# Performance work log

Measured on AMD Instinct MI355X. Metric: run time of the kernel, lower is better.

Reference implementation:

```python
import jax, jax.numpy as jnp
import numpy as np

B, C, T, F = 64, 128, 2048, 5
ALPHA, BETA = 0.5, 0.5
N = C * F  # 640 nodes


def _spatial_adjacency():
    # |i-j| <= 3 neighbors within each frequency band block (block diagonal)
    idx = np.arange(C)
    d = np.abs(idx[:, None] - idx[None, :])
    blk = ((d <= 3) & (d > 0)).astype(np.float32)
    return jnp.asarray(np.kron(np.eye(F, dtype=np.float32), blk))


A_SPATIAL = _spatial_adjacency()  # (N, N)


def setup_inputs() -> dict:
    key = jax.random.key(0)
    ks = jax.random.split(key, 5)
    names = ['delta', 'theta', 'alpha', 'beta', 'gamma']
    return {n: jax.random.normal(k, (B, C, T), dtype=jnp.float32) for n, k in zip(names, ks)}


def _strg(delta, theta, alpha, beta, gamma):
    bands = jnp.stack([delta, theta, alpha, beta, gamma], axis=1)  # (B, F, C, T)
    Bn, Fn, Cn, Tn = bands.shape

    # bandpower = unbiased variance over time (torch.var default ddof=1)
    bp = jnp.var(bands, axis=3, ddof=1)  # (B, F, C)
    bandpowers = jnp.transpose(bp, (0, 2, 1))  # (B, C, F)
    # node ordering: node f*C + ch -> bandpowers[b, ch, f] == bp[b, f, ch]
    node_features = bp.reshape(Bn, Fn * Cn, 1)

    # Pearson-style functional connectivity per batch & band (vectorized)
    mean = jnp.mean(bands, axis=3, keepdims=True)
    std = jnp.std(bands, axis=3, ddof=1, keepdims=True)  # torch.std unbiased
    xn = (bands - mean) / (std + 1e-8)
    corr = jnp.einsum('bfct,bfdt->bfcd', xn, xn) / (Tn - 1)  # (B, F, C, C)
    corr = jnp.abs(corr)
    eye = jnp.eye(Cn, dtype=corr.dtype)
    corr = corr * (1.0 - eye) + eye  # zero diag, then set diag = 1
    corr = 0.5 * (corr + jnp.swapaxes(corr, 2, 3))

    # block-diagonal assembly into full functional adjacency
    A_func = jnp.zeros((Bn, N, N), dtype=corr.dtype)
    for f in range(Fn):
        s = f * Cn
        A_func = A_func.at[:, s:s + Cn, s:s + Cn].set(corr[:, f])

    A = ALPHA * A_SPATIAL[None] + BETA * A_func  # (B, N, N)

    # symmetric degree normalization D^-1/2 A D^-1/2
    D = jnp.sum(A, axis=2)
    d_inv_sqrt = (D + 1e-8) ** -0.5
    d_inv_sqrt = jnp.where(jnp.isinf(d_inv_sqrt), 0.0, d_inv_sqrt)
    A_norm = d_inv_sqrt[:, :, None] * A * d_inv_sqrt[:, None, :]

    return A_norm, node_features, bandpowers


def reference(delta, theta, alpha, beta, gamma):
    return _strg(delta, theta, alpha, beta, gamma)
```

## Files before the change

kernel.cpp:

```cpp
#include <hip/hip_runtime.h>
#include <hip/hip_bf16.h>

#define Bn 64
#define Cn 128
#define Tn 2048
#define Fn 5
#define Nn 640
#define TCHUNK 64
#define NCHUNK 32
#define BUFBYTES (Cn * TCHUNK * 2)

typedef __attribute__((ext_vector_type(8))) short bf16x8;
typedef __attribute__((ext_vector_type(4))) short bf16x4;
typedef __attribute__((ext_vector_type(4))) float f32x4;

__device__ __forceinline__ short f2bf(float f) {
    union { float f; unsigned u; } v; v.f = f;
    unsigned r = (v.u + 0x7fffu + ((v.u >> 16) & 1u)) >> 16;
    return (short)r;
}

__device__ __forceinline__ int swz(int row, int bytecol) {
    return (row * 128 + bytecol) ^ ((row & 7) << 4);
}

__device__ __forceinline__ const float* pick_band(const float* d0, const float* d1,
                                                  const float* d2, const float* d3,
                                                  const float* d4, int f) {
    return (f == 0) ? d0 : (f == 1) ? d1 : (f == 2) ? d2 : (f == 3) ? d3 : d4;
}

__global__ __launch_bounds__(1024, 8)
void strg_mono(const float* __restrict__ d0, const float* __restrict__ d1,
               const float* __restrict__ d2, const float* __restrict__ d3,
               const float* __restrict__ d4, float* __restrict__ out)
{
    __shared__ __align__(16) char smem[Cn * Cn * 4];
    __shared__ float S_lds[Cn], diag[Cn], mrow[Cn], ivrow[Cn], Dsum[Cn], dinv_s[Cn];

    const int tid = threadIdx.x;
    const int bfid = blockIdx.x;
    const int b = bfid / Fn;
    const int f = bfid - b * Fn;
    const float* src = pick_band(d0, d1, d2, d3, d4, f) + (size_t)b * Cn * Tn;

    if (tid < Cn) { S_lds[tid] = 0.0f; Dsum[tid] = 0.0f; }

    const int srow = tid >> 4;
    const int sseg = tid & 15;
    const float* tb0 = src + (size_t)srow * Tn + sseg * 4;

    const int lane = tid & 63;
    const int w  = tid >> 6;
    const int wr = w >> 2;
    const int wc = w & 3;
    const int r0 = wr * 32;
    const int c0 = wc * 32;
    const int lg = lane >> 4;
    const int ll = lane & 15;

    f32x4 acc[2][2] = {};
    float psum[2] = {0.f, 0.f};
    float4 pfA[2], pfB[2];

    auto issueA = [&](int ch) {
        const float* cb = tb0 + ch * TCHUNK;
        #pragma unroll
        for (int i = 0; i < 2; ++i) pfA[i] = *(const float4*)(cb + (size_t)(i * 64) * Tn);
    };
    auto issueB = [&](int ch) {
        const float* cb = tb0 + ch * TCHUNK;
        #pragma unroll
        for (int i = 0; i < 2; ++i) pfB[i] = *(const float4*)(cb + (size_t)(i * 64) * Tn);
    };
    auto convA = [&](int buf) {
        char* base = smem + buf * BUFBYTES;
        #pragma unroll
        for (int i = 0; i < 2; ++i) {
            const int row = i * 64 + srow;
            float4 v = pfA[i];
            psum[i] += v.x + v.y + v.z + v.w;
            bf16x4 hh; hh[0] = f2bf(v.x); hh[1] = f2bf(v.y); hh[2] = f2bf(v.z); hh[3] = f2bf(v.w);
            *(bf16x4*)(base + swz(row, sseg * 8)) = hh;
        }
    };
    auto convB = [&](int buf) {
        char* base = smem + buf * BUFBYTES;
        #pragma unroll
        for (int i = 0; i < 2; ++i) {
            const int row = i * 64 + srow;
            float4 v = pfB[i];
            psum[i] += v.x + v.y + v.z + v.w;
            bf16x4 hh; hh[0] = f2bf(v.x); hh[1] = f2bf(v.y); hh[2] = f2bf(v.z); hh[3] = f2bf(v.w);
            *(bf16x4*)(base + swz(row, sseg * 8)) = hh;
        }
    };
    auto mfma_phase = [&](int buf) {
        const char* base = smem + buf * BUFBYTES;
        #pragma unroll
        for (int ks = 0; ks < 2; ++ks) {
            bf16x8 afr[2], bfr[2];
            #pragma unroll
            for (int m = 0; m < 2; ++m)
                afr[m] = *(const bf16x8*)(base + swz(r0 + m * 16 + ll, ks * 64 + lg * 16));
            #pragma unroll
            for (int n = 0; n < 2; ++n)
                bfr[n] = *(const bf16x8*)(base + swz(c0 + n * 16 + ll, ks * 64 + lg * 16));
            #pragma unroll
            for (int m = 0; m < 2; ++m)
                #pragma unroll
                for (int n = 0; n < 2; ++n)
                    acc[m][n] = __builtin_amdgcn_mfma_f32_16x16x32_bf16(afr[m], bfr[n], acc[m][n], 0, 0, 0);
        }
    };

    issueA(0);
    issueB(1);
    convA(0);
    issueA(2);
    asm volatile("s_waitcnt lgkmcnt(0)" ::: "memory");
    __builtin_amdgcn_s_barrier();
    __builtin_amdgcn_sched_barrier(0);

    for (int k = 0; k < NCHUNK; k += 2) {
        convB(1);
        if (k + 3 < NCHUNK) issueB(k + 3);
        mfma_phase(0);
        asm volatile("s_waitcnt lgkmcnt(0)" ::: "memory");
        __builtin_amdgcn_s_barrier();
        __builtin_amdgcn_sched_barrier(0);

        if (k + 2 < NCHUNK) {
            convA(0);
            if (k + 4 < NCHUNK) issueA(k + 4);
        }
        mfma_phase(1);
        asm volatile("s_waitcnt lgkmcnt(0)" ::: "memory");
        __builtin_amdgcn_s_barrier();
        __builtin_amdgcn_sched_barrier(0);
    }

    #pragma unroll
    for (int i = 0; i < 2; ++i) {
        float s = psum[i];
        s += __shfl_xor(s, 1);
        s += __shfl_xor(s, 2);
        s += __shfl_xor(s, 4);
        s += __shfl_xor(s, 8);
        if (ll == 0) S_lds[i * 64 + srow] = s;
    }

    #pragma unroll
    for (int m = 0; m < 2; ++m)
      #pragma unroll
      for (int n = 0; n < 2; ++n)
        #pragma unroll
        for (int e = 0; e < 4; ++e) {
            const int row = r0 + m * 16 + lg * 4 + e;
            const int col = c0 + n * 16 + ll;
            if (row == col) diag[row] = acc[m][n][e];
        }
    __syncthreads();

    if (tid < Cn) {
        const float S  = S_lds[tid];
        const float mu = S * (1.0f / Tn);
        float var = (diag[tid] - (float)Tn * mu * mu) * (1.0f / (Tn - 1));
        var = var < 0.f ? 0.f : var;
        const float sd = sqrtf(var);
        mrow[tid]  = mu;
        ivrow[tid] = 1.0f / (sd + 1e-8f);
        const size_t ofs = (size_t)Bn * Nn * Nn;
        __builtin_nontemporal_store(var, &out[ofs + (size_t)b * Nn + f * Cn + tid]);
        __builtin_nontemporal_store(var, &out[ofs + (size_t)Bn * Nn + ((size_t)b * Cn + tid) * Fn + f]);
    }
    __syncthreads();

    float* At = (float*)smem;
    {
        float mi[2][4], ii[2][4], mj[2], ij[2];
        #pragma unroll
        for (int m = 0; m < 2; ++m)
          #pragma unroll
          for (int e = 0; e < 4; ++e) {
              const int row = r0 + m * 16 + lg * 4 + e;
              mi[m][e] = mrow[row];
              ii[m][e] = ivrow[row];
          }
        #pragma unroll
        for (int n = 0; n < 2; ++n) {
            const int col = c0 + n * 16 + ll;
            mj[n] = mrow[col];
            ij[n] = ivrow[col];
        }
        const float inv = 1.0f / (Tn - 1);
        #pragma unroll
        for (int m = 0; m < 2; ++m)
          #pragma unroll
          for (int e = 0; e < 4; ++e) {
              const int row = r0 + m * 16 + lg * 4 + e;
              float s = 0.f;
              #pragma unroll
              for (int n = 0; n < 2; ++n) {
                  const int col = c0 + n * 16 + ll;
                  float c = fabsf((acc[m][n][e] - (float)Tn * mi[m][e] * mj[n])
                                  * ii[m][e] * ij[n] * inv);
                  c = (row == col) ? 1.0f : c;
                  const int d = row > col ? row - col : col - row;
                  const float spa = (d >= 1 && d <= 3) ? 1.0f : 0.0f;
                  const float a = 0.5f * (spa + c);
                  At[row * Cn + col] = a;
                  s += a;
              }
              s += __shfl_xor(s, 1);
              s += __shfl_xor(s, 2);
              s += __shfl_xor(s, 4);
              s += __shfl_xor(s, 8);
              if (ll == 0) atomicAdd(&Dsum[row], s);
          }
    }
    __syncthreads();

    if (tid < Cn) dinv_s[tid] = rsqrtf(Dsum[tid] + 1e-8f);
    __syncthreads();

    float* Ob = out + (size_t)b * Nn * Nn;
    const int fc = f * Cn;
    for (int e = 0; e < 20; ++e) {
        const int idx4 = e * 4096 + tid * 4;
        const int row = idx4 / Nn;
        const int col = idx4 - row * Nn;
        const int cl = col - fc;
        f32x4 v = {0.f, 0.f, 0.f, 0.f};
        if (cl >= 0 && cl < Cn) {
            const float dr = dinv_s[row];
            v[0] = dr * At[row * Cn + cl]     * dinv_s[cl];
            v[1] = dr * At[row * Cn + cl + 1] * dinv_s[cl + 1];
            v[2] = dr * At[row * Cn + cl + 2] * dinv_s[cl + 2];
            v[3] = dr * At[row * Cn + cl + 3] * dinv_s[cl + 3];
        }
        __builtin_nontemporal_store(v, (f32x4*)(Ob + (size_t)(fc + row) * Nn + col));
    }
}

extern "C" void kernel_launch(void* const* d_in, const int* in_sizes, int n_in,
                              void* d_out, int out_size, void* d_ws, size_t ws_size,
                              hipStream_t stream) {
    const float* d0 = (const float*)d_in[0];
    const float* d1 = (const float*)d_in[1];
    const float* d2 = (const float*)d_in[2];
    const float* d3 = (const float*)d_in[3];
    const float* d4 = (const float*)d_in[4];
    float* out = (float*)d_out;

    strg_mono<<<dim3(Bn * Fn), dim3(1024), 0, stream>>>(d0, d1, d2, d3, d4, out);
}
```

Baseline: 113.7 us.

## Replace double-buffered register prefetch pipeline with larger single-buffer chunks

Removes the double-buffered LDS and register prefetch pipeline and uses a single 256-sample time chunk per iteration, with plain __syncthreads around the load/convert and MFMA phases. Each wave now loads 8 full rows with lane-contiguous float4 reads and does a wider shuffle reduction for the row sums. This cuts the number of chunks and barriers and simplifies scheduling, but global loads are no longer overlapped with MFMA work within a block. The design relies on other resident blocks to hide load latency.

Result: slower. 131.1 us (+15.3%).

```diff
diff --git a/kernel.cpp b/kernel.cpp
--- a/kernel.cpp
+++ b/kernel.cpp
@@ -6,9 +6,9 @@
 #define Tn 2048
 #define Fn 5
 #define Nn 640
-#define TCHUNK 64
-#define NCHUNK 32
-#define BUFBYTES (Cn * TCHUNK * 2)
+#define TCHUNK 256
+#define NCHUNK 8
+#define ROWB (TCHUNK * 2)
 
 typedef __attribute__((ext_vector_type(8))) short bf16x8;
 typedef __attribute__((ext_vector_type(4))) short bf16x4;
@@ -21,7 +21,7 @@
 }
 
 __device__ __forceinline__ int swz(int row, int bytecol) {
-    return (row * 128 + bytecol) ^ ((row & 7) << 4);
+    return (row * ROWB + bytecol) ^ ((row & 7) << 4);
 }
 
 __device__ __forceinline__ const float* pick_band(const float* d0, const float* d1,
@@ -35,7 +35,7 @@
                const float* __restrict__ d2, const float* __restrict__ d3,
                const float* __restrict__ d4, float* __restrict__ out)
 {
-    __shared__ __align__(16) char smem[Cn * Cn * 4];
+    __shared__ __align__(16) char smem[Cn * ROWB];
     __shared__ float S_lds[Cn], diag[Cn], mrow[Cn], ivrow[Cn], Dsum[Cn], dinv_s[Cn];
 
     const int tid = threadIdx.x;
@@ -46,12 +46,12 @@
 
     if (tid < Cn) { S_lds[tid] = 0.0f; Dsum[tid] = 0.0f; }
 
-    const int srow = tid >> 4;
-    const int sseg = tid & 15;
-    const float* tb0 = src + (size_t)srow * Tn + sseg * 4;
-
     const int lane = tid & 63;
     const int w  = tid >> 6;
+
+    const int row_o = w * 8;
+    const float* tb0 = src + (size_t)row_o * Tn + lane * 4;
+
     const int wr = w >> 2;
     const int wc = w & 3;
     const int r0 = wr * 32;
@@ -60,94 +60,47 @@
     const int ll = lane & 15;
 
     f32x4 acc[2][2] = {};
-    float psum[2] = {0.f, 0.f};
-    float4 pfA[2], pfB[2];
-
-    auto issueA = [&](int ch) {
+    float psum[8] = {};
+
+    for (int ch = 0; ch < NCHUNK; ++ch) {
         const float* cb = tb0 + ch * TCHUNK;
         #pragma unroll
-        for (int i = 0; i < 2; ++i) pfA[i] = *(const float4*)(cb + (size_t)(i * 64) * Tn);
-    };
-    auto issueB = [&](int ch) {
-        const float* cb = tb0 + ch * TCHUNK;
-        #pragma unroll
-        for (int i = 0; i < 2; ++i) pfB[i] = *(const float4*)(cb + (size_t)(i * 64) * Tn);
-    };
-    auto convA = [&](int buf) {
-        char* base = smem + buf * BUFBYTES;
-        #pragma unroll
-        for (int i = 0; i < 2; ++i) {
-            const int row = i * 64 + srow;
-            float4 v = pfA[i];
+        for (int i = 0; i < 8; ++i) {
+            float4 v = *(const float4*)(cb + (size_t)i * Tn);
             psum[i] += v.x + v.y + v.z + v.w;
-            bf16x4 hh; hh[0] = f2bf(v.x); hh[1] = f2bf(v.y); hh[2] = f2bf(v.z); hh[3] = f2bf(v.w);
-            *(bf16x4*)(base + swz(row, sseg * 8)) = hh;
-        }
-    };
-    auto convB = [&](int buf) {
-        char* base = smem + buf * BUFBYTES;
-        #pragma unroll
-        for (int i = 0; i < 2; ++i) {
-            const int row = i * 64 + srow;
-            float4 v = pfB[i];
-            psum[i] += v.x + v.y + v.z + v.w;
-            bf16x4 hh; hh[0] = f2bf(v.x); hh[1] = f2bf(v.y); hh[2] = f2bf(v.z); hh[3] = f2bf(v.w);
-            *(bf16x4*)(base + swz(row, sseg * 8)) = hh;
-        }
-    };
-    auto mfma_phase = [&](int buf) {
-        const char* base = smem + buf * BUFBYTES;
-        #pragma unroll
-        for (int ks = 0; ks < 2; ++ks) {
+            bf16x4 h; h[0] = f2bf(v.x); h[1] = f2bf(v.y); h[2] = f2bf(v.z); h[3] = f2bf(v.w);
+            *(bf16x4*)(smem + swz(row_o + i, lane * 8)) = h;
+        }
+        __syncthreads();
+
+        #pragma unroll
+        for (int ks = 0; ks < 8; ++ks) {
             bf16x8 afr[2], bfr[2];
             #pragma unroll
             for (int m = 0; m < 2; ++m)
-                afr[m] = *(const bf16x8*)(base + swz(r0 + m * 16 + ll, ks * 64 + lg * 16));
+                afr[m] = *(const bf16x8*)(smem + swz(r0 + m * 16 + ll, ks * 64 + lg * 16));
             #pragma unroll
             for (int n = 0; n < 2; ++n)
-                bfr[n] = *(const bf16x8*)(base + swz(c0 + n * 16 + ll, ks * 64 + lg * 16));
+                bfr[n] = *(const bf16x8*)(smem + swz(c0 + n * 16 + ll, ks * 64 + lg * 16));
             #pragma unroll
             for (int m = 0; m < 2; ++m)
                 #pragma unroll
                 for (int n = 0; n < 2; ++n)
                     acc[m][n] = __builtin_amdgcn_mfma_f32_16x16x32_bf16(afr[m], bfr[n], acc[m][n], 0, 0, 0);
         }
-    };
-
-    issueA(0);
-    issueB(1);
-    convA(0);
-    issueA(2);
-    asm volatile("s_waitcnt lgkmcnt(0)" ::: "memory");
-    __builtin_amdgcn_s_barrier();
-    __builtin_amdgcn_sched_barrier(0);
-
-    for (int k = 0; k < NCHUNK; k += 2) {
-        convB(1);
-        if (k + 3 < NCHUNK) issueB(k + 3);
-        mfma_phase(0);
-        asm volatile("s_waitcnt lgkmcnt(0)" ::: "memory");
-        __builtin_amdgcn_s_barrier();
-        __builtin_amdgcn_sched_barrier(0);
-
-        if (k + 2 < NCHUNK) {
-            convA(0);
-            if (k + 4 < NCHUNK) issueA(k + 4);
-        }
-        mfma_phase(1);
-        asm volatile("s_waitcnt lgkmcnt(0)" ::: "memory");
-        __builtin_amdgcn_s_barrier();
-        __builtin_amdgcn_sched_barrier(0);
+        __syncthreads();
     }
 
     #pragma unroll
-    for (int i = 0; i < 2; ++i) {
+    for (int i = 0; i < 8; ++i) {
         float s = psum[i];
         s += __shfl_xor(s, 1);
         s += __shfl_xor(s, 2);
         s += __shfl_xor(s, 4);
         s += __shfl_xor(s, 8);
-        if (ll == 0) S_lds[i * 64 + srow] = s;
+        s += __shfl_xor(s, 16);
+        s += __shfl_xor(s, 32);
+        if (lane == 0) S_lds[row_o + i] = s;
     }
 
     #pragma unroll
```
